# Performance work log

Hardware: AMD Instinct MI355X
Metric: run time of the kernel (lower is better)

## Reference

```python
import jax, jax.numpy as jnp
import numpy as np

WIN = (8, 8)          # window height/width -> seq_len n = 64
GAMMA = 16            # channel groups (s)
BLOCKS = 1024         # num_blocks == number of windows w
GATE_DIM = 256        # dim // chunks
EPS = 1e-5


def _rel_indices(win):
    # Quadratic relative-position features [n, n, 3] = (dx, dy, dx^2+dy^2)
    w, h = win
    ind = np.arange(h)[None, :] - np.arange(w)[:, None]            # (w, h)
    indx = np.tile(ind, (h, w))                                    # (n, n)
    indy = np.repeat(np.repeat(ind, h, axis=0), w, axis=1).T       # (n, n)
    indd = indx ** 2 + indy ** 2
    return jnp.asarray(np.stack([indx, indy, indd], axis=-1), dtype=jnp.float32)


def setup_inputs() -> dict:
    key = jax.random.key(0)
    k0, k1, k2 = jax.random.split(key, 3)
    b = 4
    n = WIN[0] * WIN[1]
    return {
        "x": jax.random.normal(k0, (b, BLOCKS, n, 2 * GATE_DIM), dtype=jnp.float32),
        "norm_weight": jnp.ones((GATE_DIM,), jnp.float32),
        "norm_bias": jnp.zeros((GATE_DIM,), jnp.float32),
        "attention_centers": 0.01 * jax.random.normal(k1, (BLOCKS * GAMMA, 2), jnp.float32),
        "attention_spreads": 1.0 + 0.01 * jax.random.normal(k2, (BLOCKS * GAMMA,), jnp.float32),
        "token_proj_n_bias": jnp.zeros((BLOCKS, n, 1), jnp.float32),
    }


def reference(x, norm_weight, norm_bias, attention_centers, attention_spreads, token_proj_n_bias):
    b, w, n, d = x.shape
    # chunk into gate halves: u mixed spatially, v is the gate
    u, v = jnp.split(x, 2, axis=-1)                                # [b,w,n,gd] each
    # LayerNorm over channel dim (biased variance, as torch)
    mean = u.mean(-1, keepdims=True)
    var = u.var(-1, keepdims=True)
    u = (u - mean) * jax.lax.rsqrt(var + EPS) * norm_weight + norm_bias
    # quadratic positional weights (QuaMap.forward_qua_pos)
    mu1, mu2 = attention_centers[:, 0], attention_centers[:, 1]
    a = attention_spreads ** 2
    pos_proj = jnp.stack([a * mu1, a * mu2, -0.5 * jnp.ones_like(mu1)], axis=-1)  # [g*w, 3]
    rel = _rel_indices(WIN)                                        # [n,n,3]
    pos_score = jnp.einsum('mnd,bd->bmn', rel, pos_proj)           # [g*w, n, n]
    win_weight = jax.nn.softmax(pos_score, axis=-1)
    # rearrange '(s b) m n -> b m n s' with s=gamma
    win_weight = win_weight.reshape(GAMMA, w, n, n).transpose(1, 2, 3, 0)  # [w,m,n,s]
    # rearrange 'b w n (v s) -> b w n v s'
    vdim = u.shape[-1] // GAMMA
    uu = u.reshape(b, w, n, vdim, GAMMA)
    # windowed spatial mixing + per-window bias
    mixed = jnp.einsum('wmns,bwnvs->bwmvs', win_weight, uu)
    mixed = mixed + token_proj_n_bias[None, :, :, None, :]          # [1,w,n,1,1]
    u = mixed.reshape(b, w, n, vdim * GAMMA)
    return u * v
```

## Files before the change

### kernel.cpp

```cpp
#include <hip/hip_runtime.h>
#include <cstdint>

#if __has_builtin(__builtin_amdgcn_exp2f)
#define EXP2F(x) __builtin_amdgcn_exp2f(x)
#else
#define EXP2F(x) exp2f(x)
#endif

typedef _Float16 half8 __attribute__((ext_vector_type(8)));
typedef _Float16 half4 __attribute__((ext_vector_type(4)));
typedef float    f32x4 __attribute__((ext_vector_type(4)));


#define BARRIER() do {                                        \
    asm volatile("s_waitcnt lgkmcnt(0)" ::: "memory");        \
    __builtin_amdgcn_s_barrier();                             \
} while (0)

__global__ __launch_bounds__(512, 4) void sgating_kernel(
    const float* __restrict__ x,
    const float* __restrict__ norm_w,
    const float* __restrict__ norm_b,
    const float* __restrict__ centers,
    const float* __restrict__ spreads,
    const float* __restrict__ tbias,
    float* __restrict__ out)
{
    __shared__ __align__(16) float smem[12288];
    _Float16* Us = (_Float16*)smem;
    float*    Qm = smem + 8192;

    const int t     = threadIdx.x;
    const int wv    = t >> 6;
    const int lane  = t & 63;
    const int bw    = blockIdx.x;
    const int w_idx = bw & 1023;
    const size_t xbase = (size_t)bw * (64 * 512);
    const size_t obase = (size_t)bw * (64 * 256);

    half4 vreg[8];

    {
        const float4 w4 = *(const float4*)(norm_w + lane * 4);
        const float4 b4 = *(const float4*)(norm_b + lane * 4);
        half8 uar[4];
#pragma unroll
        for (int r = 0; r < 8; ++r) {
            const int n = r * 8 + wv;
            const float* rowp = x + xbase + (size_t)n * 512 + lane * 4;
            const float4 u  = *(const float4*)(rowp);
            const float4 vv = *(const float4*)(rowp + 256);
            vreg[r][0] = (_Float16)vv.x; vreg[r][1] = (_Float16)vv.y;
            vreg[r][2] = (_Float16)vv.z; vreg[r][3] = (_Float16)vv.w;
            float s  = u.x + u.y + u.z + u.w;
            float sq = u.x*u.x + u.y*u.y + u.z*u.z + u.w*u.w;
#pragma unroll
            for (int off = 1; off < 64; off <<= 1) {
                s  += __shfl_xor(s, off);
                sq += __shfl_xor(sq, off);
            }
            const float mean = s * (1.0f/256.0f);
            const float var  = sq * (1.0f/256.0f) - mean*mean;
            const float rstd = rsqrtf(var + 1e-5f);
            uar[0][r] = (_Float16)((u.x - mean)*rstd*w4.x + b4.x);
            uar[1][r] = (_Float16)((u.y - mean)*rstd*w4.y + b4.y);
            uar[2][r] = (_Float16)((u.z - mean)*rstd*w4.z + b4.z);
            uar[3][r] = (_Float16)((u.w - mean)*rstd*w4.w + b4.w);
        }
#pragma unroll
        for (int j = 0; j < 4; ++j) {
            const int d  = lane * 4 + j;
            const int s  = d & 15;
            const int vd = d >> 4;
            const int qb = wv ^ (vd & 7);
            *(half8*)(Us + (s << 10) + (vd << 6) + (qb << 3)) = uar[j];
        }
    }
    BARRIER();

    const int m16 = lane & 15;
    const int g   = lane >> 4;
    const float LOG2E = 1.4426950408889634f;
    const float C2    = 0.72134752044448f;
    const float mx  = (float)(m16 & 7);
    const float myb = (float)(m16 >> 3);
    const int sA = wv, sB = wv + 8;

    float bias4[4];
#pragma unroll
    for (int nt = 0; nt < 4; ++nt)
        bias4[nt] = tbias[w_idx * 64 + nt * 16 + m16];

    float    exfA[2], exfB[2];
    _Float16 exhA[2], exhB[2];
    half8 EYA_[2], EYB_[2];
    {
        const int hbA = (sA << 10) | w_idx;
        const int hbB = (sB << 10) | w_idx;
        float aq = spreads[hbA]; aq *= aq;
        const float axlA = aq * centers[2*hbA]     * LOG2E;
        const float aylA = aq * centers[2*hbA + 1] * LOG2E;
        aq = spreads[hbB]; aq *= aq;
        const float axlB = aq * centers[2*hbB]     * LOG2E;
        const float aylB = aq * centers[2*hbB + 1] * LOG2E;
#pragma unroll
        for (int kt = 0; kt < 2; ++kt) {
            const float dx = (float)(g + 4*kt) - mx;
            const float eA = EXP2F(dx * fmaf(-C2, dx, axlA));
            const float eB = EXP2F(dx * fmaf(-C2, dx, axlB));
            exfA[kt] = eA; exhA[kt] = (_Float16)eA;
            exfB[kt] = eB; exhB[kt] = (_Float16)eB;
        }
#pragma unroll
        for (int i = 0; i < 16; ++i) {
            const float dy = (float)(i - 7) + myb;
            const _Float16 eA = (i < 14) ? (_Float16)EXP2F(dy * fmaf(-C2, dy, aylA)) : (_Float16)0.f;
            const _Float16 eB = (i < 14) ? (_Float16)EXP2F(dy * fmaf(-C2, dy, aylB)) : (_Float16)0.f;
            if (i < 8) { EYA_[0][i] = eA; EYB_[0][i] = eB; }
            else       { EYA_[1][i-8] = eA; EYB_[1][i-8] = eB; }
        }
    }

#define EYAT(I) ((I) < 8 ? EYA_[0][(I)] : EYA_[1][(I)-8])
#define EYBT(I) ((I) < 8 ? EYB_[0][(I)] : EYB_[1][(I)-8])

#define CQ(NT, vOutA, vOutB) do {                                              \
    f32x4 aA = (f32x4){0.f,0.f,0.f,0.f};                                       \
    f32x4 aB = (f32x4){0.f,0.f,0.f,0.f};                                       \
    half8 eyA8, eyB8;                                                          \
    float syA = 0.f, syB = 0.f;                                                \
    _Pragma("unroll") for (int j = 0; j < 8; ++j) {                            \
        const _Float16 ea = EYAT(2*(NT)+7-j);                                  \
        const _Float16 eb = EYBT(2*(NT)+7-j);                                  \
        eyA8[j] = ea; eyB8[j] = eb;                                            \
        syA += (float)ea; syB += (float)eb;                                    \
    }                                                                          \
    _Pragma("unroll") for (int kt = 0; kt < 2; ++kt) {                         \
        const int qb = (g + 4*kt) ^ (m16 & 7);                                 \
        const half8 uA = *(const half8*)(Us + (sA<<10) + (m16<<6) + (qb<<3));  \
        const half8 uB = *(const half8*)(Us + (sB<<10) + (m16<<6) + (qb<<3));  \
        half8 wA, wB;                                                          \
        _Pragma("unroll") for (int j = 0; j < 8; ++j) {                        \
            wA[j] = eyA8[j] * exhA[kt];                                        \
            wB[j] = eyB8[j] * exhB[kt];                                        \
        }                                                                      \
        aA = __builtin_amdgcn_mfma_f32_16x16x32_f16(uA, wA, aA, 0, 0, 0);      \
        aB = __builtin_amdgcn_mfma_f32_16x16x32_f16(uB, wB, aB, 0, 0, 0);      \
    }                                                                          \
    float rA = (exfA[0] + exfA[1]) * syA;                                      \
    rA += __shfl_xor(rA, 16); rA += __shfl_xor(rA, 32);                        \
    float rB = (exfB[0] + exfB[1]) * syB;                                      \
    rB += __shfl_xor(rB, 16); rB += __shfl_xor(rB, 32);                        \
    const float iA = 1.0f / rA;                                                \
    const float iB = 1.0f / rB;                                                \
    const float bm = bias4[(NT)];                                              \
    _Pragma("unroll") for (int j = 0; j < 4; ++j) {                            \
        vOutA[j] = aA[j]*iA + bm;                                              \
        vOutB[j] = aB[j]*iB + bm;                                              \
    }                                                                          \
} while (0)

#define WRITEQ(vA_, vB_) do {                                                  \
    const int swz = (m16 & 7) << 2;                                            \
    *(f32x4*)(Qm + (m16<<8) + ((sA*16 + g*4) ^ swz)) = vA_;                    \
    *(f32x4*)(Qm + (m16<<8) + ((sB*16 + g*4) ^ swz)) = vB_;                    \
} while (0)

#define EPIK(NT, K) do {                                                       \
    const int mr  = wv + 8*(K);                                                \
    const int m   = (NT)*16 + mr;                                              \
    const int c4  = lane * 4;                                                  \
    const int vd  = c4 >> 4;                                                   \
    const int s0  = c4 & 15;                                                   \
    const int sw2 = (m & 7) << 2;                                              \
    f32x4 mxv;                                                                 \
    mxv[0] = Qm[(mr<<8) + ((((s0+0)<<4)+vd) ^ sw2)];                           \
    mxv[1] = Qm[(mr<<8) + ((((s0+1)<<4)+vd) ^ sw2)];                           \
    mxv[2] = Qm[(mr<<8) + ((((s0+2)<<4)+vd) ^ sw2)];                           \
    mxv[3] = Qm[(mr<<8) + ((((s0+3)<<4)+vd) ^ sw2)];                           \
    const half4 vh = vreg[2*(NT)+(K)];                                         \
    f32x4 o;                                                                   \
    o[0] = mxv[0] * (float)vh[0]; o[1] = mxv[1] * (float)vh[1];                \
    o[2] = mxv[2] * (float)vh[2]; o[3] = mxv[3] * (float)vh[3];                \
    __builtin_nontemporal_store(o, (f32x4*)(out + obase + m*256 + c4));        \
} while (0)

    f32x4 cA, cB, nA2, nB2;
    CQ(0, cA, cB);

    WRITEQ(cA, cB);
    BARRIER();
    CQ(1, nA2, nB2);
    EPIK(0, 0); EPIK(0, 1);
    BARRIER();
    cA = nA2; cB = nB2;

    WRITEQ(cA, cB);
    BARRIER();
    CQ(2, nA2, nB2);
    EPIK(1, 0); EPIK(1, 1);
    BARRIER();
    cA = nA2; cB = nB2;

    WRITEQ(cA, cB);
    BARRIER();
    CQ(3, nA2, nB2);
    EPIK(2, 0); EPIK(2, 1);
    BARRIER();
    cA = nA2; cB = nB2;

    WRITEQ(cA, cB);
    BARRIER();
    EPIK(3, 0); EPIK(3, 1);
}

extern "C" void kernel_launch(void* const* d_in, const int* in_sizes, int n_in,
                              void* d_out, int out_size, void* d_ws, size_t ws_size,
                              hipStream_t stream) {
    const float* x       = (const float*)d_in[0];
    const float* norm_w  = (const float*)d_in[1];
    const float* norm_b  = (const float*)d_in[2];
    const float* centers = (const float*)d_in[3];
    const float* spreads = (const float*)d_in[4];
    const float* tbias   = (const float*)d_in[5];
    float* out = (float*)d_out;

    const int nbw = in_sizes[0] / (64 * 512);
    hipLaunchKernelGGL(sgating_kernel, dim3(nbw), dim3(512), 0, stream,
                       x, norm_w, norm_b, centers, spreads, tbias, out);
}
```

Before: 156.4 us.

## Stream gate half per tile instead of holding fp16 copies in registers

The gate half v is no longer loaded up front and kept as fp16 in registers. It is now loaded in fp32 just before each output tile, issued ahead of the corresponding CQ computation so the load latency overlaps the math. This also removes an fp16 rounding of v, frees registers, and replaces the nontemporal output stores with ordinary stores. The cost is more loads issued later in the kernel and a changed ordering of barriers across the stages.

```diff
diff --git a/kernel.cpp b/kernel.cpp
--- a/kernel.cpp
+++ b/kernel.cpp
@@ -8,7 +8,6 @@
 #endif
 
 typedef _Float16 half8 __attribute__((ext_vector_type(8)));
-typedef _Float16 half4 __attribute__((ext_vector_type(4)));
 typedef float    f32x4 __attribute__((ext_vector_type(4)));
 
 
@@ -38,8 +37,6 @@
     const size_t xbase = (size_t)bw * (64 * 512);
     const size_t obase = (size_t)bw * (64 * 256);
 
-    half4 vreg[8];
-
     {
         const float4 w4 = *(const float4*)(norm_w + lane * 4);
         const float4 b4 = *(const float4*)(norm_b + lane * 4);
@@ -47,11 +44,7 @@
 #pragma unroll
         for (int r = 0; r < 8; ++r) {
             const int n = r * 8 + wv;
-            const float* rowp = x + xbase + (size_t)n * 512 + lane * 4;
-            const float4 u  = *(const float4*)(rowp);
-            const float4 vv = *(const float4*)(rowp + 256);
-            vreg[r][0] = (_Float16)vv.x; vreg[r][1] = (_Float16)vv.y;
-            vreg[r][2] = (_Float16)vv.z; vreg[r][3] = (_Float16)vv.w;
+            const float4 u = *(const float4*)(x + xbase + (size_t)n * 512 + lane * 4);
             float s  = u.x + u.y + u.z + u.w;
             float sq = u.x*u.x + u.y*u.y + u.z*u.z + u.w*u.w;
 #pragma unroll
@@ -76,7 +69,6 @@
             *(half8*)(Us + (s << 10) + (vd << 6) + (qb << 3)) = uar[j];
         }
     }
-    BARRIER();
 
     const int m16 = lane & 15;
     const int g   = lane >> 4;
@@ -166,7 +158,12 @@
     *(f32x4*)(Qm + (m16<<8) + ((sB*16 + g*4) ^ swz)) = vB_;                    \
 } while (0)
 
-#define EPIK(NT, K) do {                                                       \
+#define VLOAD(NT, V0, V1) do {                                                 \
+    V0 = *(const f32x4*)(x + xbase + (size_t)(16*(NT)+wv)*512 + 256 + lane*4); \
+    V1 = *(const f32x4*)(x + xbase + (size_t)(16*(NT)+8+wv)*512 + 256 + lane*4);\
+} while (0)
+
+#define EPI1(NT, K, VH) do {                                                   \
     const int mr  = wv + 8*(K);                                                \
     const int m   = (NT)*16 + mr;                                              \
     const int c4  = lane * 4;                                                  \
@@ -178,40 +175,47 @@
     mxv[1] = Qm[(mr<<8) + ((((s0+1)<<4)+vd) ^ sw2)];                           \
     mxv[2] = Qm[(mr<<8) + ((((s0+2)<<4)+vd) ^ sw2)];                           \
     mxv[3] = Qm[(mr<<8) + ((((s0+3)<<4)+vd) ^ sw2)];                           \
-    const half4 vh = vreg[2*(NT)+(K)];                                         \
     f32x4 o;                                                                   \
-    o[0] = mxv[0] * (float)vh[0]; o[1] = mxv[1] * (float)vh[1];                \
-    o[2] = mxv[2] * (float)vh[2]; o[3] = mxv[3] * (float)vh[3];                \
-    __builtin_nontemporal_store(o, (f32x4*)(out + obase + m*256 + c4));        \
-} while (0)
+    o[0] = mxv[0]*(VH)[0]; o[1] = mxv[1]*(VH)[1];                              \
+    o[2] = mxv[2]*(VH)[2]; o[3] = mxv[3]*(VH)[3];                              \
+    *(f32x4*)(out + obase + m*256 + c4) = o;                                   \
+} while (0)
+
+#define EPI2(NT, VA, VB) do { EPI1(NT, 0, VA); EPI1(NT, 1, VB); } while (0)
+
+    f32x4 v0, v1, v2, v3, v4, v5, v6, v7;
+    VLOAD(0, v0, v1);
+    BARRIER();
 
     f32x4 cA, cB, nA2, nB2;
     CQ(0, cA, cB);
-
     WRITEQ(cA, cB);
     BARRIER();
+
+    VLOAD(1, v2, v3);
     CQ(1, nA2, nB2);
-    EPIK(0, 0); EPIK(0, 1);
-    BARRIER();
-    cA = nA2; cB = nB2;
-
+    EPI2(0, v0, v1);
+    BARRIER();
+    WRITEQ(nA2, nB2);
+    BARRIER();
+
+    VLOAD(2, v4, v5);
+    CQ(2, cA, cB);
+    EPI2(1, v2, v3);
+    BARRIER();
     WRITEQ(cA, cB);
     BARRIER();
-    CQ(2, nA2, nB2);
-    EPIK(1, 0); EPIK(1, 1);
-    BARRIER();
-    cA = nA2; cB = nB2;
-
-    WRITEQ(cA, cB);
-    BARRIER();
+
+    VLOAD(3, v6, v7);
     CQ(3, nA2, nB2);
-    EPIK(2, 0); EPIK(2, 1);
-    BARRIER();
-    cA = nA2; cB = nB2;
-
-    WRITEQ(cA, cB);
-    BARRIER();
-    EPIK(3, 0); EPIK(3, 1);
+    EPI2(2, v4, v5);
+    BARRIER();
+    WRITEQ(nA2, nB2);
+    BARRIER();
+
+    EPI2(3, v6, v7);
+
+    asm volatile("s_waitcnt vmcnt(0)" ::: "memory");
 }
 
 extern "C" void kernel_launch(void* const* d_in, const int* in_sizes, int n_in,
```

Measured after the change: 153.6 us. No clear change (-1.7%).
